# Optimization experiments

Measured on AMD Instinct MI355X. Metric: run time of the kernel, lower is better.

The kernel has to match this reference:

```python
import jax, jax.numpy as jnp
import numpy as np

N = 50000       # nodes
E = 800000      # edges (avg degree 16)
DIN = 64        # input feature dim
HID = 128       # hidden dim (= per-head out_channels in GATConv)
HEADS = 4
G = 64          # graphs in the batch
NC = 8          # num classes
EPS = 1e-5      # BatchNorm eps
NEG_SLOPE = 0.2 # GAT leaky_relu slope


def setup_inputs():
    key = jax.random.key(0)
    it = iter(jax.random.split(key, 40))
    def p(shape, s=0.05):
        return jax.random.normal(next(it), shape, jnp.float32) * s
    x = jax.random.normal(next(it), (N, DIN), jnp.float32)
    edge_index = jax.random.randint(next(it), (2, E), 0, N)
    batch = jnp.sort(jax.random.randint(next(it), (N,), 0, G))
    inp = dict(x=x, edge_index=edge_index, batch=batch)
    inp["s0_Wl"] = p((DIN, HID)); inp["s0_Wr"] = p((DIN, HID)); inp["s0_b"] = p((HID,))
    inp["s1_Wl"] = p((HID, HID)); inp["s1_Wr"] = p((HID, HID)); inp["s1_b"] = p((HID,))
    inp["bn_g"] = 1.0 + p((4, HID)); inp["bn_b"] = p((4, HID))
    inp["bn_m"] = p((4, HID)); inp["bn_v"] = 0.5 + jax.random.uniform(next(it), (4, HID))
    inp["prelu_a"] = 0.25 + p((4, HID))
    for i in range(2):
        inp[f"g{i}_W"] = p((HID, HEADS * HID))
        inp[f"g{i}_as"] = p((HEADS, HID)); inp[f"g{i}_ad"] = p((HEADS, HID))
        inp[f"g{i}_bias"] = p((HID,))
    inp["idp_W"] = p((3, HID, HID)); inp["idp_b"] = p((3, HID)); inp["idp_a"] = 0.25 + p((2, HID))
    inp["cls_W"] = p((HID, NC)); inp["cls_b"] = p((NC,))
    return inp


def _bn(x, g, b, m, v):
    return (x - m) * jax.lax.rsqrt(v + EPS) * g + b


def _prelu(x, a):
    return jnp.where(x >= 0, x, a * x)


def _sage(x, src, dst, Wl, Wr, b):
    # PyG SAGEConv: lin_l(mean_{j->i} x_j) + lin_r(x_i)
    s = jax.ops.segment_sum(x[src], dst, num_segments=N)
    cnt = jax.ops.segment_sum(jnp.ones((src.shape[0],), x.dtype), dst, num_segments=N)
    agg = s / jnp.maximum(cnt, 1.0)[:, None]
    return agg @ Wl + b + x @ Wr


def _gat(x, src, dst, W, a_src, a_dst, bias):
    # src/dst already include self-loops (PyG GATConv default). concat=False -> mean over heads.
    xw = (x @ W).reshape(N, HEADS, HID)               # [N,H,C]
    es = jnp.einsum('nhc,hc->nh', xw, a_src)          # [N,H]
    ed = jnp.einsum('nhc,hc->nh', xw, a_dst)
    e = jax.nn.leaky_relu(es[src] + ed[dst], NEG_SLOPE)   # [E2,H]
    m = jax.lax.stop_gradient(jax.ops.segment_max(e, dst, num_segments=N))
    ex = jnp.exp(e - m[dst])
    den = jax.ops.segment_sum(ex, dst, num_segments=N)
    alpha = ex / den[dst]                                  # [E2,H] softmax per destination
    # per-head scatter to keep peak memory ~[E2,C] instead of [E2,H,C]
    heads = [jax.ops.segment_sum(alpha[:, h:h + 1] * xw[src, h, :], dst, num_segments=N)
             for h in range(HEADS)]
    return jnp.stack(heads, 1).mean(1) + bias


def _model(x, edge_index, batch, s0_Wl, s0_Wr, s0_b, s1_Wl, s1_Wr, s1_b,
           bn_g, bn_b, bn_m, bn_v, prelu_a,
           g0_W, g0_as, g0_ad, g0_bias, g1_W, g1_as, g1_ad, g1_bias,
           idp_W, idp_b, idp_a, cls_W, cls_b):
    src, dst = edge_index[0], edge_index[1]
    h = _sage(x, src, dst, s0_Wl, s0_Wr, s0_b)
    h = _prelu(_bn(h, bn_g[0], bn_b[0], bn_m[0], bn_v[0]), prelu_a[0])
    h = _sage(h, src, dst, s1_Wl, s1_Wr, s1_b)
    h = _prelu(_bn(h, bn_g[1], bn_b[1], bn_m[1], bn_v[1]), prelu_a[1])
    loop = jnp.arange(N)
    src2 = jnp.concatenate([src, loop]); dst2 = jnp.concatenate([dst, loop])
    h = _gat(h, src2, dst2, g0_W, g0_as, g0_ad, g0_bias)
    h = _prelu(_bn(h, bn_g[2], bn_b[2], bn_m[2], bn_v[2]), prelu_a[2])
    h = _gat(h, src2, dst2, g1_W, g1_as, g1_ad, g1_bias)
    h = _prelu(_bn(h, bn_g[3], bn_b[3], bn_m[3], bn_v[3]), prelu_a[3])
    # IDP MLP (dropout inactive in eval)
    h = _prelu(h @ idp_W[0] + idp_b[0], idp_a[0])
    h = _prelu(h @ idp_W[1] + idp_b[1], idp_a[1])
    h = h @ idp_W[2] + idp_b[2]
    # global mean pool per graph
    sums = jax.ops.segment_sum(h, batch, num_segments=G)
    cnt = jax.ops.segment_sum(jnp.ones((N,), h.dtype), batch, num_segments=G)
    gemb = sums / jnp.maximum(cnt, 1.0)[:, None]
    return gemb @ cls_W + cls_b


def reference(x, edge_index, batch, s0_Wl, s0_Wr, s0_b, s1_Wl, s1_Wr, s1_b,
              bn_g, bn_b, bn_m, bn_v, prelu_a,
              g0_W, g0_as, g0_ad, g0_bias, g1_W, g1_as, g1_ad, g1_bias,
              idp_W, idp_b, idp_a, cls_W, cls_b):
    return _model(x, edge_index, batch, s0_Wl, s0_Wr, s0_b, s1_Wl, s1_Wr, s1_b,
                  bn_g, bn_b, bn_m, bn_v, prelu_a,
                  g0_W, g0_as, g0_ad, g0_bias, g1_W, g1_as, g1_ad, g1_bias,
                  idp_W, idp_b, idp_a, cls_W, cls_b)
```

## Files before the change

kernel.cpp:

```cpp
#include <hip/hip_runtime.h>
#include <hip/hip_bf16.h>
#include <math.h>

#define N_NODES 50000
#define N_EDGES 800000
#define DIN     64
#define HID     128
#define HEADS   4
#define NGRAPH  64
#define NCLS    8
#define EPSB    1e-5f
#define SLOPE   0.2f
#define PSEG    16
#define MAXC4   64
#define FP8S    16.0f
#define FP8SI   (0.25f / FP8S)

#define SCB     256
#define NSB     ((N_NODES + SCB - 1) / SCB)

#define MPAD    (N_NODES + 64)
#define TPAD    136

typedef __hip_bfloat16 bf16;
typedef __attribute__((ext_vector_type(8))) short short8;
typedef __attribute__((ext_vector_type(4))) float f32x4;
typedef __attribute__((ext_vector_type(2))) float f32x2;

__device__ __forceinline__ float b2f(bf16 v) { return __bfloat162float(v); }
__device__ __forceinline__ bf16  f2b(float v) { return __float2bfloat16(v); }
__device__ __forceinline__ float lo_f(unsigned v) {
    unsigned u = v << 16; return __builtin_bit_cast(float, u);
}
__device__ __forceinline__ float hi_f(unsigned v) {
    unsigned u = v & 0xffff0000u; return __builtin_bit_cast(float, u);
}
__device__ __forceinline__ unsigned packbf(float lo, float hi) {
    unsigned l = (unsigned)__builtin_bit_cast(unsigned short, __float2bfloat16(lo));
    unsigned h = (unsigned)__builtin_bit_cast(unsigned short, __float2bfloat16(hi));
    return (h << 16) | l;
}

__global__ void k_count_bounds(const int* __restrict__ ei, int* __restrict__ deg,
                               const int* __restrict__ batch, int* __restrict__ gstart) {
    int e = blockIdx.x * 256 + threadIdx.x;
    if (e < N_EDGES) atomicAdd(&deg[ei[N_EDGES + e]], 1);
    int i = e;
    if (i < N_NODES) {
        int b = batch[i];
        int prev = (i == 0) ? -1 : batch[i - 1];
        for (int g = prev + 1; g <= b; ++g) gstart[g] = i;
        if (i == N_NODES - 1)
            for (int g = b + 1; g <= NGRAPH; ++g) gstart[g] = N_NODES;
    }
}

__global__ void k_scan1(const int* __restrict__ deg, int* __restrict__ row_off,
                        int* __restrict__ bsum) {
    __shared__ int sm[SCB];
    int b = blockIdx.x, t = threadIdx.x;
    int i = b * SCB + t;
    int v = (i < N_NODES) ? deg[i] : 0;
    sm[t] = v;
    __syncthreads();
    for (int off = 1; off < SCB; off <<= 1) {
        int x = (t >= off) ? sm[t - off] : 0;
        __syncthreads();
        sm[t] += x;
        __syncthreads();
    }
    if (i < N_NODES) row_off[i + 1] = sm[t];
    if (t == SCB - 1) bsum[b] = sm[t];
}

__global__ void k_scan2(const int* __restrict__ bsum, int* __restrict__ boff) {
    __shared__ int sm[SCB];
    int t = threadIdx.x;
    int v = (t < NSB) ? bsum[t] : 0;
    sm[t] = v;
    __syncthreads();
    for (int off = 1; off < SCB; off <<= 1) {
        int x = (t >= off) ? sm[t - off] : 0;
        __syncthreads();
        sm[t] += x;
        __syncthreads();
    }
    boff[t] = sm[t] - v;
}

__global__ void k_scan3(int* __restrict__ row_off, const int* __restrict__ boff) {
    int i = blockIdx.x * 256 + threadIdx.x;
    if (i == 0) row_off[0] = 0;
    if (i < N_NODES) row_off[i + 1] += boff[i >> 8];
}

__global__ void k_fill(const int* __restrict__ ei, const int* __restrict__ row_off,
                       int* __restrict__ cursor, int* __restrict__ col) {
    int e = blockIdx.x * 256 + threadIdx.x;
    if (e < N_EDGES) {
        int s = ei[e], d = ei[N_EDGES + e];
        int pos = atomicAdd(&cursor[d], 1);
        col[row_off[d] + pos] = s;
    }
}

__global__ void k_prep(const float* __restrict__ s0Wl, const float* __restrict__ s0Wr,
                       const float* __restrict__ s1Wl, const float* __restrict__ s1Wr,
                       const float* __restrict__ g0W,  const float* __restrict__ g1W,
                       const float* __restrict__ idpW,
                       bf16* __restrict__ s0t, bf16* __restrict__ s1t,
                       bf16* __restrict__ g0t, bf16* __restrict__ g1t,
                       bf16* __restrict__ idpt) {
    int t = blockIdx.x * 256 + threadIdx.x;
    if (t < 16384) { int n = t >> 7, k = t & 127;
        s0t[t] = f2b(k < 64 ? s0Wl[k * 128 + n] : s0Wr[(k - 64) * 128 + n]); return; }
    t -= 16384;
    if (t < 32768) { int n = t >> 8, k = t & 255;
        s1t[t] = f2b(k < 128 ? s1Wl[k * 128 + n] : s1Wr[(k - 128) * 128 + n]); return; }
    t -= 32768;
    if (t < 65536) { int n = t >> 7, k = t & 127; g0t[t] = f2b(g0W[k * 512 + n]); return; }
    t -= 65536;
    if (t < 65536) { int n = t >> 7, k = t & 127; g1t[t] = f2b(g1W[k * 512 + n]); return; }
    t -= 65536;
    if (t < 49152) { int l = t >> 14, r = t & 16383; int n = r >> 7, k = r & 127;
        idpt[t] = f2b(idpW[l * 16384 + k * 128 + n]); }
}

__global__ __launch_bounds__(256) void k_sage_agg_f32(
        const float* __restrict__ xin, const int* __restrict__ row_off,
        const int* __restrict__ col, bf16* __restrict__ acat) {
    __shared__ int sCol[4][MAXC4];
    int w = threadIdx.x >> 6, lane = threadIdx.x & 63;
    int i = blockIdx.x * 4 + w;
    int s0 = row_off[i], s1 = row_off[i + 1];
    float acc = 0.f;
    for (int c0 = s0; c0 < s1; c0 += MAXC4) {
        int cnt = min(MAXC4, s1 - c0);
        if (lane < cnt) sCol[w][lane] = col[c0 + lane];
        for (int e = 0; e < cnt; ++e)
            acc += xin[(size_t)sCol[w][e] * DIN + lane];
    }
    acat[(size_t)i * (2 * DIN) + lane]       = f2b(acc / fmaxf((float)(s1 - s0), 1.0f));
    acat[(size_t)i * (2 * DIN) + DIN + lane] = f2b(xin[(size_t)i * DIN + lane]);
}

__global__ __launch_bounds__(256) void k_sage_agg_bf(
        const bf16* __restrict__ xin, const int* __restrict__ row_off,
        const int* __restrict__ col, bf16* __restrict__ acat) {
    __shared__ int sCol[4][MAXC4];
    int w = threadIdx.x >> 6, lane = threadIdx.x & 63;
    int i = blockIdx.x * 4 + w;
    int s0 = row_off[i], s1 = row_off[i + 1];
    const unsigned* xb = (const unsigned*)xin;
    float a0 = 0.f, a1 = 0.f;
    for (int c0 = s0; c0 < s1; c0 += MAXC4) {
        int cnt = min(MAXC4, s1 - c0);
        if (lane < cnt) sCol[w][lane] = col[c0 + lane];
        for (int e = 0; e < cnt; ++e) {
            unsigned v = xb[(size_t)sCol[w][e] * (HID / 2) + lane];
            a0 += lo_f(v); a1 += hi_f(v);
        }
    }
    float inv = 1.0f / fmaxf((float)(s1 - s0), 1.0f);
    unsigned* ao = (unsigned*)acat;
    ao[(size_t)i * HID + lane]              = packbf(a0 * inv, a1 * inv);
    ao[(size_t)i * HID + (HID / 2) + lane]  = xb[(size_t)i * (HID / 2) + lane];
}

template <int K, int NT, int EPI>
__global__ __launch_bounds__(256) void k_gemm(
        const bf16* __restrict__ A, const bf16* __restrict__ Bt, void* __restrict__ Cp,
        int M, int Nc,
        const float* __restrict__ bias, const float* __restrict__ bng,
        const float* __restrict__ bnb,  const float* __restrict__ bnm,
        const float* __restrict__ bnv,  const float* __restrict__ pa,
        const float* __restrict__ asrc, const float* __restrict__ adst,
        float* __restrict__ es, float* __restrict__ ed) {
    int wave = threadIdx.x >> 6, lane = threadIdx.x & 63;
    int ln = lane & 15, q = lane >> 4;
    int m0 = blockIdx.x * 64 + wave * 16;
    int n0 = blockIdx.y * (NT * 16);
    const bf16* arow = A + (size_t)(m0 + ln) * K + q * 8;

    f32x4 acc[NT];
#pragma unroll
    for (int t = 0; t < NT; ++t) acc[t] = (f32x4){0.f, 0.f, 0.f, 0.f};

#pragma unroll
    for (int k = 0; k < K; k += 32) {
        short8 a = *(const short8*)(const void*)(arow + k);
#pragma unroll
        for (int t = 0; t < NT; ++t) {
            short8 b = *(const short8*)(const void*)(Bt + (size_t)(n0 + t * 16 + ln) * K + k + q * 8);
            acc[t] = __builtin_amdgcn_mfma_f32_16x16x32_bf16(a, b, acc[t], 0, 0, 0);
        }
    }

    if (EPI != 4) {
        bf16* C = (bf16*)Cp;
#pragma unroll
        for (int t = 0; t < NT; ++t) {
            int cidx = n0 + t * 16 + ln;
            float bi = bias[cidx];
            float g = bng[cidx], bb = bnb[cidx], mm = bnm[cidx];
            float iv = rsqrtf(bnv[cidx] + EPSB), al = pa[cidx];
#pragma unroll
            for (int r = 0; r < 4; ++r) {
                int mr = m0 + q * 4 + r;
                if (mr < M) {
                    float v = acc[t][r] + bi;
                    v = (v - mm) * iv * g + bb;
                    v = v >= 0.f ? v : al * v;
                    C[(size_t)mr * Nc + cidx] = f2b(v);
                }
            }
        }
    } else {
        unsigned char* C8 = (unsigned char*)Cp;
#pragma unroll
        for (int t = 0; t < NT; ++t) {
            int cidx = n0 + t * 16 + ln;
#pragma unroll
            for (int r = 0; r < 4; ++r) {
                int mr = m0 + q * 4 + r;
                if (mr < M) {
                    int enc = __builtin_amdgcn_cvt_pk_fp8_f32(acc[t][r] * FP8S, 0.f, 0, false);
                    C8[(size_t)mr * 512 + cidx] = (unsigned char)(enc & 0xff);
                }
            }
        }
        int head = blockIdx.y;
        float asv[NT], adv[NT];
#pragma unroll
        for (int t = 0; t < NT; ++t) {
            asv[t] = asrc[head * HID + t * 16 + ln];
            adv[t] = adst[head * HID + t * 16 + ln];
        }
#pragma unroll
        for (int r = 0; r < 4; ++r) {
            float ps = 0.f, pd = 0.f;
#pragma unroll
            for (int t = 0; t < NT; ++t) { ps += acc[t][r] * asv[t]; pd += acc[t][r] * adv[t]; }
#pragma unroll
            for (int off = 1; off < 16; off <<= 1) {
                ps += __shfl_xor(ps, off, 16);
                pd += __shfl_xor(pd, off, 16);
            }
            int mr = m0 + q * 4 + r;
            if (ln == 0 && mr < M) {
                es[mr * HEADS + head] = ps;
                ed[mr * HEADS + head] = pd;
            }
        }
    }
}

__global__ __launch_bounds__(256) void k_mlp3(
        const bf16* __restrict__ A,
        const bf16* __restrict__ W0t, const bf16* __restrict__ W1t,
        const bf16* __restrict__ W2t,
        const float* __restrict__ b0, const float* __restrict__ a0,
        const float* __restrict__ b1, const float* __restrict__ a1,
        const float* __restrict__ b2,
        bf16* __restrict__ outp, int M) {
    __shared__ bf16 tile[4][16][TPAD];
    int wave = threadIdx.x >> 6, lane = threadIdx.x & 63;
    int ln = lane & 15, q = lane >> 4;
    int m0 = blockIdx.x * 64 + wave * 16;
    bf16* myt = &tile[wave][0][0];

    f32x4 acc[8];
#pragma unroll
    for (int t = 0; t < 8; ++t) acc[t] = (f32x4){0.f, 0.f, 0.f, 0.f};
    {
        const bf16* arow = A + (size_t)(m0 + ln) * HID + q * 8;
#pragma unroll
        for (int k = 0; k < HID; k += 32) {
            short8 a = *(const short8*)(const void*)(arow + k);
#pragma unroll
            for (int t = 0; t < 8; ++t) {
                short8 b = *(const short8*)(const void*)(W0t + (size_t)(t * 16 + ln) * HID + k + q * 8);
                acc[t] = __builtin_amdgcn_mfma_f32_16x16x32_bf16(a, b, acc[t], 0, 0, 0);
            }
        }
#pragma unroll
        for (int t = 0; t < 8; ++t) {
            int c = t * 16 + ln;
            float bi = b0[c], al = a0[c];
#pragma unroll
            for (int r = 0; r < 4; ++r) {
                float v = acc[t][r] + bi;
                v = v >= 0.f ? v : al * v;
                myt[(q * 4 + r) * TPAD + c] = f2b(v);
            }
        }
    }
    {
#pragma unroll
        for (int t = 0; t < 8; ++t) acc[t] = (f32x4){0.f, 0.f, 0.f, 0.f};
#pragma unroll
        for (int k = 0; k < HID; k += 32) {
            short8 a = *(const short8*)(const void*)(&myt[ln * TPAD + k + q * 8]);
#pragma unroll
            for (int t = 0; t < 8; ++t) {
                short8 b = *(const short8*)(const void*)(W1t + (size_t)(t * 16 + ln) * HID + k + q * 8);
                acc[t] = __builtin_amdgcn_mfma_f32_16x16x32_bf16(a, b, acc[t], 0, 0, 0);
            }
        }
#pragma unroll
        for (int t = 0; t < 8; ++t) {
            int c = t * 16 + ln;
            float bi = b1[c], al = a1[c];
#pragma unroll
            for (int r = 0; r < 4; ++r) {
                float v = acc[t][r] + bi;
                v = v >= 0.f ? v : al * v;
                myt[(q * 4 + r) * TPAD + c] = f2b(v);
            }
        }
    }
    {
#pragma unroll
        for (int t = 0; t < 8; ++t) acc[t] = (f32x4){0.f, 0.f, 0.f, 0.f};
#pragma unroll
        for (int k = 0; k < HID; k += 32) {
            short8 a = *(const short8*)(const void*)(&myt[ln * TPAD + k + q * 8]);
#pragma unroll
            for (int t = 0; t < 8; ++t) {
                short8 b = *(const short8*)(const void*)(W2t + (size_t)(t * 16 + ln) * HID + k + q * 8);
                acc[t] = __builtin_amdgcn_mfma_f32_16x16x32_bf16(a, b, acc[t], 0, 0, 0);
            }
        }
#pragma unroll
        for (int t = 0; t < 8; ++t) {
            int c = t * 16 + ln;
            float bi = b2[c];
#pragma unroll
            for (int r = 0; r < 4; ++r) {
                int mr = m0 + q * 4 + r;
                if (mr < M) outp[(size_t)mr * HID + c] = f2b(acc[t][r] + bi);
            }
        }
    }
}

__global__ __launch_bounds__(256) void k_gat_agg(
        const unsigned char* __restrict__ xw8, const float* __restrict__ es,
        const float* __restrict__ ed, const int* __restrict__ row_off,
        const int* __restrict__ col, const float* __restrict__ bias,
        const float* __restrict__ bng, const float* __restrict__ bnb,
        const float* __restrict__ bnm, const float* __restrict__ bnv,
        const float* __restrict__ pa,
        bf16* __restrict__ out) {
    __shared__ __align__(16) float sEx[4][MAXC4][HEADS];
    __shared__ int sCol[4][MAXC4];
    int w = threadIdx.x >> 6;
    int lane = threadIdx.x & 63;
    int i = blockIdx.x * 4 + w;
    int h = lane >> 4;
    const uint2*  xw2 = (const uint2*)xw8;
    const float4* es4 = (const float4*)es;
    float4 edi = ((const float4*)ed)[i];

    int s0 = row_off[i], s1 = row_off[i + 1];
    float den0 = 0.f, den1 = 0.f, den2 = 0.f, den3 = 0.f;
    float a[8];
#pragma unroll
    for (int j = 0; j < 8; ++j) a[j] = 0.f;

    {
        float4 ev = es4[i];
        float e0 = ev.x + edi.x; e0 = e0 >= 0.f ? e0 : SLOPE * e0; float x0 = expf(e0);
        float e1 = ev.y + edi.y; e1 = e1 >= 0.f ? e1 : SLOPE * e1; float x1 = expf(e1);
        float e2 = ev.z + edi.z; e2 = e2 >= 0.f ? e2 : SLOPE * e2; float x2 = expf(e2);
        float e3 = ev.w + edi.w; e3 = e3 >= 0.f ? e3 : SLOPE * e3; float x3 = expf(e3);
        if (lane == 0) { den0 = x0; den1 = x1; den2 = x2; den3 = x3; }
        float ex = h == 0 ? x0 : h == 1 ? x1 : h == 2 ? x2 : x3;
        uint2 v = xw2[(size_t)i * 64 + lane];
        f32x2 p0 = __builtin_amdgcn_cvt_pk_f32_fp8((int)v.x, false);
        f32x2 p1 = __builtin_amdgcn_cvt_pk_f32_fp8((int)v.x, true);
        f32x2 p2 = __builtin_amdgcn_cvt_pk_f32_fp8((int)v.y, false);
        f32x2 p3 = __builtin_amdgcn_cvt_pk_f32_fp8((int)v.y, true);
        a[0] += ex * p0.x; a[1] += ex * p0.y;
        a[2] += ex * p1.x; a[3] += ex * p1.y;
        a[4] += ex * p2.x; a[5] += ex * p2.y;
        a[6] += ex * p3.x; a[7] += ex * p3.y;
    }
    for (int c0 = s0; c0 < s1; c0 += MAXC4) {
        int cnt = min(MAXC4, s1 - c0);
        if (lane < cnt) {
            int s = col[c0 + lane];
            float4 ev = es4[s];
            float e0 = ev.x + edi.x; e0 = e0 >= 0.f ? e0 : SLOPE * e0; float x0 = expf(e0);
            float e1 = ev.y + edi.y; e1 = e1 >= 0.f ? e1 : SLOPE * e1; float x1 = expf(e1);
            float e2 = ev.z + edi.z; e2 = e2 >= 0.f ? e2 : SLOPE * e2; float x2 = expf(e2);
            float e3 = ev.w + edi.w; e3 = e3 >= 0.f ? e3 : SLOPE * e3; float x3 = expf(e3);
            den0 += x0; den1 += x1; den2 += x2; den3 += x3;
            sCol[w][lane] = s;
            f32x4 xv = {x0, x1, x2, x3};
            *(f32x4*)(&sEx[w][lane][0]) = xv;
        }
        for (int e = 0; e < cnt; ++e) {
            float ex = sEx[w][e][h];
            int s = sCol[w][e];
            uint2 v = xw2[(size_t)s * 64 + lane];
            f32x2 p0 = __builtin_amdgcn_cvt_pk_f32_fp8((int)v.x, false);
            f32x2 p1 = __builtin_amdgcn_cvt_pk_f32_fp8((int)v.x, true);
            f32x2 p2 = __builtin_amdgcn_cvt_pk_f32_fp8((int)v.y, false);
            f32x2 p3 = __builtin_amdgcn_cvt_pk_f32_fp8((int)v.y, true);
            a[0] += ex * p0.x; a[1] += ex * p0.y;
            a[2] += ex * p1.x; a[3] += ex * p1.y;
            a[4] += ex * p2.x; a[5] += ex * p2.y;
            a[6] += ex * p3.x; a[7] += ex * p3.y;
        }
    }
    for (int off = 1; off < 64; off <<= 1) {
        den0 += __shfl_xor(den0, off, 64);
        den1 += __shfl_xor(den1, off, 64);
        den2 += __shfl_xor(den2, off, 64);
        den3 += __shfl_xor(den3, off, 64);
    }
    float den = h == 0 ? den0 : h == 1 ? den1 : h == 2 ? den2 : den3;
    float inv = 1.0f / den;
    float m[8];
#pragma unroll
    for (int j = 0; j < 8; ++j) m[j] = a[j] * inv;
#pragma unroll
    for (int j = 0; j < 8; ++j) {
        m[j] += __shfl_xor(m[j], 16, 64);
        m[j] += __shfl_xor(m[j], 32, 64);
    }
    if (lane < 16) {
        int cb = lane * 8;
        float r[8];
#pragma unroll
        for (int j = 0; j < 8; ++j) {
            int c = cb + j;
            float v = FP8SI * m[j] + bias[c];
            v = (v - bnm[c]) * rsqrtf(bnv[c] + EPSB) * bng[c] + bnb[c];
            float al = pa[c];
            r[j] = v >= 0.f ? v : al * v;
        }
        uint4 o;
        o.x = packbf(r[0], r[1]); o.y = packbf(r[2], r[3]);
        o.z = packbf(r[4], r[5]); o.w = packbf(r[6], r[7]);
        ((uint4*)out)[(size_t)i * 16 + lane] = o;
    }
}

__global__ void k_pool(const bf16* __restrict__ h, const int* __restrict__ gstart,
                       float* __restrict__ pool) {
    int g = blockIdx.x, s = blockIdx.y;
    int c = threadIdx.x;
    int b0 = gstart[g], b1 = gstart[g + 1];
    int len = b1 - b0;
    if (len <= 0) return;
    int per = (len + PSEG - 1) / PSEG;
    int r0 = b0 + s * per;
    int r1 = min(r0 + per, b1);
    if (r0 >= r1) return;
    const unsigned* hb = (const unsigned*)h;
    float a0 = 0.f, a1 = 0.f;
    for (int i = r0; i < r1; ++i) {
        unsigned v = hb[(size_t)i * (HID / 2) + c];
        a0 += lo_f(v); a1 += hi_f(v);
    }
    atomicAdd(&pool[g * HID + 2 * c], a0);
    atomicAdd(&pool[g * HID + 2 * c + 1], a1);
}

__global__ void k_cls(const float* __restrict__ pool, const int* __restrict__ gstart,
                      const float* __restrict__ W, const float* __restrict__ b,
                      float* __restrict__ out) {
    int t = threadIdx.x;
    int g = t / NCLS, n = t % NCLS;
    float ic = 1.0f / fmaxf((float)(gstart[g + 1] - gstart[g]), 1.0f);
    float acc = b[n];
    for (int k = 0; k < HID; ++k)
        acc += pool[g * HID + k] * ic * W[k * NCLS + n];
    out[g * NCLS + n] = acc;
}

extern "C" void kernel_launch(void* const* d_in, const int* in_sizes, int n_in,
                              void* d_out, int out_size, void* d_ws, size_t ws_size,
                              hipStream_t stream) {
    const float* x      = (const float*)d_in[0];
    const int*   ei     = (const int*)d_in[1];
    const int*   batch  = (const int*)d_in[2];
    const float* s0_Wl  = (const float*)d_in[3];
    const float* s0_Wr  = (const float*)d_in[4];
    const float* s0_b   = (const float*)d_in[5];
    const float* s1_Wl  = (const float*)d_in[6];
    const float* s1_Wr  = (const float*)d_in[7];
    const float* s1_b   = (const float*)d_in[8];
    const float* bn_g   = (const float*)d_in[9];
    const float* bn_b   = (const float*)d_in[10];
    const float* bn_m   = (const float*)d_in[11];
    const float* bn_v   = (const float*)d_in[12];
    const float* pre_a  = (const float*)d_in[13];
    const float* g0_W   = (const float*)d_in[14];
    const float* g0_as  = (const float*)d_in[15];
    const float* g0_ad  = (const float*)d_in[16];
    const float* g0_bias= (const float*)d_in[17];
    const float* g1_W   = (const float*)d_in[18];
    const float* g1_as  = (const float*)d_in[19];
    const float* g1_ad  = (const float*)d_in[20];
    const float* g1_bias= (const float*)d_in[21];
    const float* idp_W  = (const float*)d_in[22];
    const float* idp_b  = (const float*)d_in[23];
    const float* idp_a  = (const float*)d_in[24];
    const float* cls_W  = (const float*)d_in[25];
    const float* cls_b  = (const float*)d_in[26];
    float* out = (float*)d_out;

    char* p = (char*)d_ws;
    auto alloc = [&](size_t bytes) -> void* {
        void* r = (void*)p;
        p += (bytes + 255) & ~(size_t)255;
        return r;
    };
    int*   degcur  = (int*)alloc((size_t)2 * N_NODES * 4);
    int*   deg     = degcur;
    int*   cursor  = degcur + N_NODES;
    int*   row_off = (int*)alloc((size_t)(N_NODES + 1) * 4);
    int*   col     = (int*)alloc((size_t)N_EDGES * 4);
    int*   gstart  = (int*)alloc((size_t)(NGRAPH + 1) * 4);
    int*   bsum    = (int*)alloc((size_t)SCB * 4);
    int*   boff    = (int*)alloc((size_t)SCB * 4);
    float* es      = (float*)alloc((size_t)N_NODES * HEADS * 4);
    float* edv     = (float*)alloc((size_t)N_NODES * HEADS * 4);
    float* pool    = (float*)alloc((size_t)NGRAPH * HID * 4);
    bf16*  hA      = (bf16*)alloc((size_t)MPAD * HID * 2);
    bf16*  hB      = (bf16*)alloc((size_t)MPAD * HID * 2);
    void*  u       = alloc((size_t)MPAD * 512);
    bf16*  acat0   = (bf16*)u;
    bf16*  acat1   = (bf16*)u;
    unsigned char* xw8 = (unsigned char*)u;
    bf16*  s0t     = (bf16*)alloc((size_t)128 * 128 * 2);
    bf16*  s1t     = (bf16*)alloc((size_t)128 * 256 * 2);
    bf16*  g0t     = (bf16*)alloc((size_t)512 * 128 * 2);
    bf16*  g1t     = (bf16*)alloc((size_t)512 * 128 * 2);
    bf16*  idpt    = (bf16*)alloc((size_t)3 * 128 * 128 * 2);

    hipMemsetAsync(degcur, 0, (size_t)2 * N_NODES * 4, stream);
    hipMemsetAsync(pool, 0, (size_t)NGRAPH * HID * 4, stream);

    k_prep<<<(229376 + 255) / 256, 256, 0, stream>>>(s0_Wl, s0_Wr, s1_Wl, s1_Wr,
                                                     g0_W, g1_W, idp_W,
                                                     s0t, s1t, g0t, g1t, idpt);
    k_count_bounds<<<(N_EDGES + 255) / 256, 256, 0, stream>>>(ei, deg, batch, gstart);
    k_scan1<<<NSB, SCB, 0, stream>>>(deg, row_off, bsum);
    k_scan2<<<1, SCB, 0, stream>>>(bsum, boff);
    k_scan3<<<(N_NODES + 255) / 256, 256, 0, stream>>>(row_off, boff);
    k_fill<<<(N_EDGES + 255) / 256, 256, 0, stream>>>(ei, row_off, cursor, col);

    const int MB = (N_NODES + 63) / 64;

    k_sage_agg_f32<<<N_NODES / 4, 256, 0, stream>>>(x, row_off, col, acat0);
    k_gemm<128, 8, 1><<<dim3(MB, 1), 256, 0, stream>>>(
        acat0, s0t, hA, N_NODES, HID,
        s0_b, bn_g + 0 * HID, bn_b + 0 * HID, bn_m + 0 * HID, bn_v + 0 * HID, pre_a + 0 * HID,
        nullptr, nullptr, nullptr, nullptr);

    k_sage_agg_bf<<<N_NODES / 4, 256, 0, stream>>>(hA, row_off, col, acat1);
    k_gemm<256, 8, 1><<<dim3(MB, 1), 256, 0, stream>>>(
        acat1, s1t, hB, N_NODES, HID,
        s1_b, bn_g + 1 * HID, bn_b + 1 * HID, bn_m + 1 * HID, bn_v + 1 * HID, pre_a + 1 * HID,
        nullptr, nullptr, nullptr, nullptr);

    k_gemm<128, 8, 4><<<dim3(MB, 4), 256, 0, stream>>>(
        hB, g0t, xw8, N_NODES, HEADS * HID,
        nullptr, nullptr, nullptr, nullptr, nullptr, nullptr,
        g0_as, g0_ad, es, edv);
    k_gat_agg<<<N_NODES / 4, 256, 0, stream>>>(
        xw8, es, edv, row_off, col, g0_bias,
        bn_g + 2 * HID, bn_b + 2 * HID, bn_m + 2 * HID, bn_v + 2 * HID, pre_a + 2 * HID, hA);

    k_gemm<128, 8, 4><<<dim3(MB, 4), 256, 0, stream>>>(
        hA, g1t, xw8, N_NODES, HEADS * HID,
        nullptr, nullptr, nullptr, nullptr, nullptr, nullptr,
        g1_as, g1_ad, es, edv);
    k_gat_agg<<<N_NODES / 4, 256, 0, stream>>>(
        xw8, es, edv, row_off, col, g1_bias,
        bn_g + 3 * HID, bn_b + 3 * HID, bn_m + 3 * HID, bn_v + 3 * HID, pre_a + 3 * HID, hB);

    k_mlp3<<<MB, 256, 0, stream>>>(
        hB, idpt + 0 * 16384, idpt + 1 * 16384, idpt + 2 * 16384,
        idp_b + 0 * HID, idp_a + 0 * HID,
        idp_b + 1 * HID, idp_a + 1 * HID,
        idp_b + 2 * HID, hA, N_NODES);

    k_pool<<<dim3(NGRAPH, PSEG), 64, 0, stream>>>(hA, gstart, pool);
    k_cls<<<1, NGRAPH * NCLS, 0, stream>>>(pool, gstart, cls_W, cls_b, out);
}
```

Before: 667.6 us.

## Gather bf16/fp8 copies in SAGE layers, fuse prep kernels and pool+classifier

The input x is converted to bf16 inside a merged prep kernel that also does degree counting and graph bounds, so the first SAGE gather reads half the bytes. The first SAGE GEMM also writes an fp8-scaled copy of its output, which the second SAGE gather reads, halving gather traffic again at a precision cost. GAT aggregation uses packed f32x2 FMAs. Pooling and the classifier are fused into one kernel, which drops the atomics and the memset. Together these remove launches and gather bandwidth, but add extra stores for the xbf and fp8 copies and lose accuracy from fp8.

```diff
diff --git a/kernel.cpp b/kernel.cpp
--- a/kernel.cpp
+++ b/kernel.cpp
@@ -11,7 +11,6 @@
 #define NCLS    8
 #define EPSB    1e-5f
 #define SLOPE   0.2f
-#define PSEG    16
 #define MAXC4   64
 #define FP8S    16.0f
 #define FP8SI   (0.25f / FP8S)
@@ -41,17 +40,44 @@
     return (h << 16) | l;
 }
 
-__global__ void k_count_bounds(const int* __restrict__ ei, int* __restrict__ deg,
-                               const int* __restrict__ batch, int* __restrict__ gstart) {
-    int e = blockIdx.x * 256 + threadIdx.x;
-    if (e < N_EDGES) atomicAdd(&deg[ei[N_EDGES + e]], 1);
-    int i = e;
-    if (i < N_NODES) {
-        int b = batch[i];
-        int prev = (i == 0) ? -1 : batch[i - 1];
-        for (int g = prev + 1; g <= b; ++g) gstart[g] = i;
-        if (i == N_NODES - 1)
-            for (int g = b + 1; g <= NGRAPH; ++g) gstart[g] = N_NODES;
+#define PREP_W  229376
+#define PREP_X  (N_NODES * DIN)
+#define PREP_T  (PREP_W + PREP_X + N_EDGES)
+__global__ void k_prep(const float* __restrict__ s0Wl, const float* __restrict__ s0Wr,
+                       const float* __restrict__ s1Wl, const float* __restrict__ s1Wr,
+                       const float* __restrict__ g0W,  const float* __restrict__ g1W,
+                       const float* __restrict__ idpW, const float* __restrict__ x,
+                       const int* __restrict__ ei,     const int* __restrict__ batch,
+                       bf16* __restrict__ s0t, bf16* __restrict__ s1t,
+                       bf16* __restrict__ g0t, bf16* __restrict__ g1t,
+                       bf16* __restrict__ idpt, bf16* __restrict__ xbf,
+                       int* __restrict__ deg, int* __restrict__ gstart) {
+    int t = blockIdx.x * 256 + threadIdx.x;
+    if (t < 16384) { int n = t >> 7, k = t & 127;
+        s0t[t] = f2b(k < 64 ? s0Wl[k * 128 + n] : s0Wr[(k - 64) * 128 + n]); return; }
+    t -= 16384;
+    if (t < 32768) { int n = t >> 8, k = t & 255;
+        s1t[t] = f2b(k < 128 ? s1Wl[k * 128 + n] : s1Wr[(k - 128) * 128 + n]); return; }
+    t -= 32768;
+    if (t < 65536) { int n = t >> 7, k = t & 127; g0t[t] = f2b(g0W[k * 512 + n]); return; }
+    t -= 65536;
+    if (t < 65536) { int n = t >> 7, k = t & 127; g1t[t] = f2b(g1W[k * 512 + n]); return; }
+    t -= 65536;
+    if (t < 49152) { int l = t >> 14, r = t & 16383; int n = r >> 7, k = r & 127;
+        idpt[t] = f2b(idpW[l * 16384 + k * 128 + n]); return; }
+    t -= 49152;
+    if (t < PREP_X) { xbf[t] = f2b(x[t]); return; }
+    t -= PREP_X;
+    if (t < N_EDGES) {
+        atomicAdd(&deg[ei[N_EDGES + t]], 1);
+        int i = t;
+        if (i < N_NODES) {
+            int b = batch[i];
+            int prev = (i == 0) ? -1 : batch[i - 1];
+            for (int g = prev + 1; g <= b; ++g) gstart[g] = i;
+            if (i == N_NODES - 1)
+                for (int g = b + 1; g <= NGRAPH; ++g) gstart[g] = N_NODES;
+        }
     }
 }
 
@@ -104,73 +130,55 @@
     }
 }
 
-__global__ void k_prep(const float* __restrict__ s0Wl, const float* __restrict__ s0Wr,
-                       const float* __restrict__ s1Wl, const float* __restrict__ s1Wr,
-                       const float* __restrict__ g0W,  const float* __restrict__ g1W,
-                       const float* __restrict__ idpW,
-                       bf16* __restrict__ s0t, bf16* __restrict__ s1t,
-                       bf16* __restrict__ g0t, bf16* __restrict__ g1t,
-                       bf16* __restrict__ idpt) {
-    int t = blockIdx.x * 256 + threadIdx.x;
-    if (t < 16384) { int n = t >> 7, k = t & 127;
-        s0t[t] = f2b(k < 64 ? s0Wl[k * 128 + n] : s0Wr[(k - 64) * 128 + n]); return; }
-    t -= 16384;
-    if (t < 32768) { int n = t >> 8, k = t & 255;
-        s1t[t] = f2b(k < 128 ? s1Wl[k * 128 + n] : s1Wr[(k - 128) * 128 + n]); return; }
-    t -= 32768;
-    if (t < 65536) { int n = t >> 7, k = t & 127; g0t[t] = f2b(g0W[k * 512 + n]); return; }
-    t -= 65536;
-    if (t < 65536) { int n = t >> 7, k = t & 127; g1t[t] = f2b(g1W[k * 512 + n]); return; }
-    t -= 65536;
-    if (t < 49152) { int l = t >> 14, r = t & 16383; int n = r >> 7, k = r & 127;
-        idpt[t] = f2b(idpW[l * 16384 + k * 128 + n]); }
-}
-
-__global__ __launch_bounds__(256) void k_sage_agg_f32(
-        const float* __restrict__ xin, const int* __restrict__ row_off,
-        const int* __restrict__ col, bf16* __restrict__ acat) {
+__global__ __launch_bounds__(256) void k_sage_agg0(
+        const bf16* __restrict__ xbf, const float* __restrict__ x,
+        const int* __restrict__ row_off, const int* __restrict__ col,
+        bf16* __restrict__ acat) {
     __shared__ int sCol[4][MAXC4];
     int w = threadIdx.x >> 6, lane = threadIdx.x & 63;
     int i = blockIdx.x * 4 + w;
     int s0 = row_off[i], s1 = row_off[i + 1];
+    const unsigned short* xs = (const unsigned short*)xbf;
     float acc = 0.f;
     for (int c0 = s0; c0 < s1; c0 += MAXC4) {
         int cnt = min(MAXC4, s1 - c0);
         if (lane < cnt) sCol[w][lane] = col[c0 + lane];
         for (int e = 0; e < cnt; ++e)
-            acc += xin[(size_t)sCol[w][e] * DIN + lane];
+            acc += lo_f((unsigned)xs[(size_t)sCol[w][e] * DIN + lane]);
     }
     acat[(size_t)i * (2 * DIN) + lane]       = f2b(acc / fmaxf((float)(s1 - s0), 1.0f));
-    acat[(size_t)i * (2 * DIN) + DIN + lane] = f2b(xin[(size_t)i * DIN + lane]);
-}
-
-__global__ __launch_bounds__(256) void k_sage_agg_bf(
-        const bf16* __restrict__ xin, const int* __restrict__ row_off,
-        const int* __restrict__ col, bf16* __restrict__ acat) {
+    acat[(size_t)i * (2 * DIN) + DIN + lane] = f2b(x[(size_t)i * DIN + lane]);
+}
+
+__global__ __launch_bounds__(256) void k_sage_agg1(
+        const unsigned char* __restrict__ hA8, const bf16* __restrict__ hA,
+        const int* __restrict__ row_off, const int* __restrict__ col,
+        bf16* __restrict__ acat) {
     __shared__ int sCol[4][MAXC4];
     int w = threadIdx.x >> 6, lane = threadIdx.x & 63;
     int i = blockIdx.x * 4 + w;
     int s0 = row_off[i], s1 = row_off[i + 1];
-    const unsigned* xb = (const unsigned*)xin;
-    float a0 = 0.f, a1 = 0.f;
+    const unsigned short* h8 = (const unsigned short*)hA8;
+    f32x2 acc = {0.f, 0.f};
     for (int c0 = s0; c0 < s1; c0 += MAXC4) {
         int cnt = min(MAXC4, s1 - c0);
         if (lane < cnt) sCol[w][lane] = col[c0 + lane];
         for (int e = 0; e < cnt; ++e) {
-            unsigned v = xb[(size_t)sCol[w][e] * (HID / 2) + lane];
-            a0 += lo_f(v); a1 += hi_f(v);
-        }
-    }
-    float inv = 1.0f / fmaxf((float)(s1 - s0), 1.0f);
+            f32x2 p = __builtin_amdgcn_cvt_pk_f32_fp8(
+                (int)(unsigned)h8[(size_t)sCol[w][e] * (HID / 2) + lane], false);
+            acc += p;
+        }
+    }
+    float inv = 1.0f / (fmaxf((float)(s1 - s0), 1.0f) * FP8S);
     unsigned* ao = (unsigned*)acat;
-    ao[(size_t)i * HID + lane]              = packbf(a0 * inv, a1 * inv);
-    ao[(size_t)i * HID + (HID / 2) + lane]  = xb[(size_t)i * (HID / 2) + lane];
+    ao[(size_t)i * HID + lane]             = packbf(acc.x * inv, acc.y * inv);
+    ao[(size_t)i * HID + (HID / 2) + lane] = ((const unsigned*)hA)[(size_t)i * (HID / 2) + lane];
 }
 
 template <int K, int NT, int EPI>
 __global__ __launch_bounds__(256) void k_gemm(
         const bf16* __restrict__ A, const bf16* __restrict__ Bt, void* __restrict__ Cp,
-        int M, int Nc,
+        unsigned char* __restrict__ C8s, int M, int Nc,
         const float* __restrict__ bias, const float* __restrict__ bng,
         const float* __restrict__ bnb,  const float* __restrict__ bnm,
         const float* __restrict__ bnv,  const float* __restrict__ pa,
@@ -212,6 +220,10 @@
                     v = (v - mm) * iv * g + bb;
                     v = v >= 0.f ? v : al * v;
                     C[(size_t)mr * Nc + cidx] = f2b(v);
+                    if (EPI == 5) {
+                        int enc = __builtin_amdgcn_cvt_pk_fp8_f32(v * FP8S, 0.f, 0, false);
+                        C8s[(size_t)mr * HID + cidx] = (unsigned char)(enc & 0xff);
+                    }
                 }
             }
         }
@@ -364,9 +376,7 @@
 
     int s0 = row_off[i], s1 = row_off[i + 1];
     float den0 = 0.f, den1 = 0.f, den2 = 0.f, den3 = 0.f;
-    float a[8];
-#pragma unroll
-    for (int j = 0; j < 8; ++j) a[j] = 0.f;
+    f32x2 a01 = {0.f, 0.f}, a23 = {0.f, 0.f}, a45 = {0.f, 0.f}, a67 = {0.f, 0.f};
 
     {
         float4 ev = es4[i];
@@ -376,15 +386,12 @@
         float e3 = ev.w + edi.w; e3 = e3 >= 0.f ? e3 : SLOPE * e3; float x3 = expf(e3);
         if (lane == 0) { den0 = x0; den1 = x1; den2 = x2; den3 = x3; }
         float ex = h == 0 ? x0 : h == 1 ? x1 : h == 2 ? x2 : x3;
+        f32x2 ex2 = {ex, ex};
         uint2 v = xw2[(size_t)i * 64 + lane];
-        f32x2 p0 = __builtin_amdgcn_cvt_pk_f32_fp8((int)v.x, false);
-        f32x2 p1 = __builtin_amdgcn_cvt_pk_f32_fp8((int)v.x, true);
-        f32x2 p2 = __builtin_amdgcn_cvt_pk_f32_fp8((int)v.y, false);
-        f32x2 p3 = __builtin_amdgcn_cvt_pk_f32_fp8((int)v.y, true);
-        a[0] += ex * p0.x; a[1] += ex * p0.y;
-        a[2] += ex * p1.x; a[3] += ex * p1.y;
-        a[4] += ex * p2.x; a[5] += ex * p2.y;
-        a[6] += ex * p3.x; a[7] += ex * p3.y;
+        a01 = __builtin_elementwise_fma(__builtin_amdgcn_cvt_pk_f32_fp8((int)v.x, false), ex2, a01);
+        a23 = __builtin_elementwise_fma(__builtin_amdgcn_cvt_pk_f32_fp8((int)v.x, true),  ex2, a23);
+        a45 = __builtin_elementwise_fma(__builtin_amdgcn_cvt_pk_f32_fp8((int)v.y, false), ex2, a45);
+        a67 = __builtin_elementwise_fma(__builtin_amdgcn_cvt_pk_f32_fp8((int)v.y, true),  ex2, a67);
     }
     for (int c0 = s0; c0 < s1; c0 += MAXC4) {
         int cnt = min(MAXC4, s1 - c0);
@@ -402,16 +409,13 @@
         }
         for (int e = 0; e < cnt; ++e) {
             float ex = sEx[w][e][h];
+            f32x2 ex2 = {ex, ex};
             int s = sCol[w][e];
             uint2 v = xw2[(size_t)s * 64 + lane];
-            f32x2 p0 = __builtin_amdgcn_cvt_pk_f32_fp8((int)v.x, false);
-            f32x2 p1 = __builtin_amdgcn_cvt_pk_f32_fp8((int)v.x, true);
-            f32x2 p2 = __builtin_amdgcn_cvt_pk_f32_fp8((int)v.y, false);
-            f32x2 p3 = __builtin_amdgcn_cvt_pk_f32_fp8((int)v.y, true);
-            a[0] += ex * p0.x; a[1] += ex * p0.y;
-            a[2] += ex * p1.x; a[3] += ex * p1.y;
-            a[4] += ex * p2.x; a[5] += ex * p2.y;
-            a[6] += ex * p3.x; a[7] += ex * p3.y;
+            a01 = __builtin_elementwise_fma(__builtin_amdgcn_cvt_pk_f32_fp8((int)v.x, false), ex2, a01);
+            a23 = __builtin_elementwise_fma(__builtin_amdgcn_cvt_pk_f32_fp8((int)v.x, true),  ex2, a23);
+            a45 = __builtin_elementwise_fma(__builtin_amdgcn_cvt_pk_f32_fp8((int)v.y, false), ex2, a45);
+            a67 = __builtin_elementwise_fma(__builtin_amdgcn_cvt_pk_f32_fp8((int)v.y, true),  ex2, a67);
         }
     }
     for (int off = 1; off < 64; off <<= 1) {
@@ -422,9 +426,8 @@
     }
     float den = h == 0 ? den0 : h == 1 ? den1 : h == 2 ? den2 : den3;
     float inv = 1.0f / den;
-    float m[8];
-#pragma unroll
-    for (int j = 0; j < 8; ++j) m[j] = a[j] * inv;
+    float m[8] = {a01.x * inv, a01.y * inv, a23.x * inv, a23.y * inv,
+                  a45.x * inv, a45.y * inv, a67.x * inv, a67.y * inv};
 #pragma unroll
     for (int j = 0; j < 8; ++j) {
         m[j] += __shfl_xor(m[j], 16, 64);
@@ -448,37 +451,35 @@
     }
 }
 
-__global__ void k_pool(const bf16* __restrict__ h, const int* __restrict__ gstart,
-                       float* __restrict__ pool) {
-    int g = blockIdx.x, s = blockIdx.y;
-    int c = threadIdx.x;
+__global__ __launch_bounds__(256) void k_poolcls(
+        const bf16* __restrict__ h, const int* __restrict__ gstart,
+        const float* __restrict__ W, const float* __restrict__ b,
+        float* __restrict__ out) {
+    __shared__ float sO[4][HID];
+    __shared__ float gemb[HID];
+    int g = blockIdx.x;
+    int w = threadIdx.x >> 6, lane = threadIdx.x & 63;
     int b0 = gstart[g], b1 = gstart[g + 1];
-    int len = b1 - b0;
-    if (len <= 0) return;
-    int per = (len + PSEG - 1) / PSEG;
-    int r0 = b0 + s * per;
-    int r1 = min(r0 + per, b1);
-    if (r0 >= r1) return;
     const unsigned* hb = (const unsigned*)h;
     float a0 = 0.f, a1 = 0.f;
-    for (int i = r0; i < r1; ++i) {
-        unsigned v = hb[(size_t)i * (HID / 2) + c];
+    for (int r = b0 + w; r < b1; r += 4) {
+        unsigned v = hb[(size_t)r * (HID / 2) + lane];
         a0 += lo_f(v); a1 += hi_f(v);
     }
-    atomicAdd(&pool[g * HID + 2 * c], a0);
-    atomicAdd(&pool[g * HID + 2 * c + 1], a1);
-}
-
-__global__ void k_cls(const float* __restrict__ pool, const int* __restrict__ gstart,
-                      const float* __restrict__ W, const float* __restrict__ b,
-                      float* __restrict__ out) {
+    sO[w][2 * lane]     = a0;
+    sO[w][2 * lane + 1] = a1;
+    __syncthreads();
     int t = threadIdx.x;
-    int g = t / NCLS, n = t % NCLS;
-    float ic = 1.0f / fmaxf((float)(gstart[g + 1] - gstart[g]), 1.0f);
-    float acc = b[n];
-    for (int k = 0; k < HID; ++k)
-        acc += pool[g * HID + k] * ic * W[k * NCLS + n];
-    out[g * NCLS + n] = acc;
+    if (t < HID) {
+        float s = sO[0][t] + sO[1][t] + sO[2][t] + sO[3][t];
+        gemb[t] = s / fmaxf((float)(b1 - b0), 1.0f);
+    }
+    __syncthreads();
+    if (t < NCLS) {
+        float acc = b[t];
+        for (int k = 0; k < HID; ++k) acc += gemb[k] * W[k * NCLS + t];
+        out[g * NCLS + t] = acc;
+    }
 }
 
 extern "C" void kernel_launch(void* const* d_in, const int* in_sizes, int n_in,
@@ -529,9 +530,10 @@
     int*   boff    = (int*)alloc((size_t)SCB * 4);
     float* es      = (float*)alloc((size_t)N_NODES * HEADS * 4);
     float* edv     = (float*)alloc((size_t)N_NODES * HEADS * 4);
-    float* pool    = (float*)alloc((size_t)NGRAPH * HID * 4);
     bf16*  hA      = (bf16*)alloc((size_t)MPAD * HID * 2);
     bf16*  hB      = (bf16*)alloc((size_t)MPAD * HID * 2);
+    bf16*  xbf     = (bf16*)alloc((size_t)N_NODES * DIN * 2);
+    unsigned char* hA8 = (unsigned char*)alloc((size_t)MPAD * HID);
     void*  u       = alloc((size_t)MPAD * 512);
     bf16*  acat0   = (bf16*)u;
     bf16*  acat1   = (bf16*)u;
@@ -543,12 +545,10 @@
     bf16*  idpt    = (bf16*)alloc((size_t)3 * 128 * 128 * 2);
 
     hipMemsetAsync(degcur, 0, (size_t)2 * N_NODES * 4, stream);
-    hipMemsetAsync(pool, 0, (size_t)NGRAPH * HID * 4, stream);
-
-    k_prep<<<(229376 + 255) / 256, 256, 0, stream>>>(s0_Wl, s0_Wr, s1_Wl, s1_Wr,
-                                                     g0_W, g1_W, idp_W,
-                                                     s0t, s1t, g0t, g1t, idpt);
-    k_count_bounds<<<(N_EDGES + 255) / 256, 256, 0, stream>>>(ei, deg, batch, gstart);
+
+    k_prep<<<(PREP_T + 255) / 256, 256, 0, stream>>>(
+        s0_Wl, s0_Wr, s1_Wl, s1_Wr, g0_W, g1_W, idp_W, x, ei, batch,
+        s0t, s1t, g0t, g1t, idpt, xbf, deg, gstart);
     k_scan1<<<NSB, SCB, 0, stream>>>(deg, row_off, bsum);
     k_scan2<<<1, SCB, 0, stream>>>(bsum, boff);
     k_scan3<<<(N_NODES + 255) / 256, 256, 0, stream>>>(row_off, boff);
@@ -556,20 +556,20 @@
 
     const int MB = (N_NODES + 63) / 64;
 
-    k_sage_agg_f32<<<N_NODES / 4, 256, 0, stream>>>(x, row_off, col, acat0);
-    k_gemm<128, 8, 1><<<dim3(MB, 1), 256, 0, stream>>>(
-        acat0, s0t, hA, N_NODES, HID,
+    k_sage_agg0<<<N_NODES / 4, 256, 0, stream>>>(xbf, x, row_off, col, acat0);
+    k_gemm<128, 8, 5><<<dim3(MB, 1), 256, 0, stream>>>(
+        acat0, s0t, hA, hA8, N_NODES, HID,
         s0_b, bn_g + 0 * HID, bn_b + 0 * HID, bn_m + 0 * HID, bn_v + 0 * HID, pre_a + 0 * HID,
         nullptr, nullptr, nullptr, nullptr);
 
-    k_sage_agg_bf<<<N_NODES / 4, 256, 0, stream>>>(hA, row_off, col, acat1);
+    k_sage_agg1<<<N_NODES / 4, 256, 0, stream>>>(hA8, hA, row_off, col, acat1);
     k_gemm<256, 8, 1><<<dim3(MB, 1), 256, 0, stream>>>(
-        acat1, s1t, hB, N_NODES, HID,
+        acat1, s1t, hB, nullptr, N_NODES, HID,
         s1_b, bn_g + 1 * HID, bn_b + 1 * HID, bn_m + 1 * HID, bn_v + 1 * HID, pre_a + 1 * HID,
         nullptr, nullptr, nullptr, nullptr);
 
     k_gemm<128, 8, 4><<<dim3(MB, 4), 256, 0, stream>>>(
-        hB, g0t, xw8, N_NODES, HEADS * HID,
+        hB, g0t, xw8, nullptr, N_NODES, HEADS * HID,
         nullptr, nullptr, nullptr, nullptr, nullptr, nullptr,
         g0_as, g0_ad, es, edv);
     k_gat_agg<<<N_NODES / 4, 256, 0, stream>>>(
@@ -577,7 +577,7 @@
         bn_g + 2 * HID, bn_b + 2 * HID, bn_m + 2 * HID, bn_v + 2 * HID, pre_a + 2 * HID, hA);
 
     k_gemm<128, 8, 4><<<dim3(MB, 4), 256, 0, stream>>>(
-        hA, g1t, xw8, N_NODES, HEADS * HID,
+        hA, g1t, xw8, nullptr, N_NODES, HEADS * HID,
         nullptr, nullptr, nullptr, nullptr, nullptr, nullptr,
         g1_as, g1_ad, es, edv);
     k_gat_agg<<<N_NODES / 4, 256, 0, stream>>>(
@@ -590,6 +590,5 @@
         idp_b + 1 * HID, idp_a + 1 * HID,
         idp_b + 2 * HID, hA, N_NODES);
 
-    k_pool<<<dim3(NGRAPH, PSEG), 64, 0, stream>>>(hA, gstart, pool);
-    k_cls<<<1, NGRAPH * NCLS, 0, stream>>>(pool, gstart, cls_W, cls_b, out);
-}
+    k_poolcls<<<NGRAPH, 256, 0, stream>>>(hA, gstart, cls_W, cls_b, out);
+}
```

Result: slower. 698.7 us (+4.6%).
